# Kernel optimization log

Measured on AMD Instinct MI355X. Metric: run time of the kernel, lower is better.

The kernel has to match this reference:

```python
import jax, jax.numpy as jnp
import numpy as np

B, S, E, H = 4, 2048, 1024, 16
D = E // H          # head_dim = 64
FF = 3 * E          # feedforward_expansion = 3
EPS = 1.1920929e-07  # torch fp32 RMSNorm default eps (finfo.eps)


def rmsnorm(x, w):
    ms = jnp.mean(jnp.square(x), axis=-1, keepdims=True)
    return x * jax.lax.rsqrt(ms + EPS) * w


def setup_inputs() -> dict:
    key = jax.random.key(0)
    ks = jax.random.split(key, 12)
    s = 0.02
    return {
        "x": jax.random.normal(ks[0], (B, S, E), dtype=jnp.float32),
        "mask": jnp.ones((B, 1, 1, S), dtype=jnp.int32),
        "Wq": jax.random.normal(ks[1], (E, E), dtype=jnp.float32) * s,
        "bq": jnp.zeros((E,), dtype=jnp.float32),
        "Wkv": jax.random.normal(ks[2], (E, 2 * E), dtype=jnp.float32) * s,
        "bkv": jnp.zeros((2 * E,), dtype=jnp.float32),
        "Wo": jax.random.normal(ks[3], (E, E), dtype=jnp.float32) * s,
        "bo": jnp.zeros((E,), dtype=jnp.float32),
        "norm1_w": jnp.ones((E,), dtype=jnp.float32),
        "norm3_w": jnp.ones((E,), dtype=jnp.float32),
        "W1": jax.random.normal(ks[4], (E, FF), dtype=jnp.float32) * s,
        "b1": jnp.zeros((FF,), dtype=jnp.float32),
        "W2": jax.random.normal(ks[5], (FF, E), dtype=jnp.float32) * s,
        "b2": jnp.zeros((E,), dtype=jnp.float32),
    }


def attention(xn, mask, Wq, bq, Wkv, bkv, Wo, bo):
    q = xn @ Wq + bq                         # [B,S,E]
    kv = xn @ Wkv + bkv                      # [B,S,2E]
    k, v = jnp.split(kv, 2, axis=-1)
    q = q.reshape(B, S, H, D).transpose(0, 2, 1, 3)   # [B,H,S,D]
    k = k.reshape(B, S, H, D).transpose(0, 2, 1, 3)
    v = v.reshape(B, S, H, D).transpose(0, 2, 1, 3)
    scores = jnp.einsum("bhqd,bhkd->bhqk", q, k) / jnp.sqrt(jnp.float32(D))
    scores = jnp.where(mask == 0, -jnp.inf, scores)
    probs = jax.nn.softmax(scores, axis=-1)
    out = jnp.einsum("bhqk,bhkd->bhqd", probs, v)     # [B,H,S,D]
    out = out.transpose(0, 2, 1, 3).reshape(B, S, E)
    return out @ Wo + bo


def reference(x, mask, Wq, bq, Wkv, bkv, Wo, bo, norm1_w, norm3_w, W1, b1, W2, b2):
    # self-attention sublayer (pre-norm, residual; dropout = identity in eval)
    xn = rmsnorm(x, norm1_w)
    x = x + attention(xn, mask, Wq, bq, Wkv, bkv, Wo, bo)
    # feedforward sublayer: Linear -> exact GELU -> Linear
    xn = rmsnorm(x, norm3_w)
    h = jax.nn.gelu(xn @ W1 + b1, approximate=False)
    x = x + (h @ W2 + b2)
    return x
```

## Files before the change

### kernel.cpp

```cpp
#include <hip/hip_runtime.h>
#include <stdint.h>
#include <math.h>

typedef unsigned short u16;
typedef __attribute__((ext_vector_type(8))) short short8;
typedef __attribute__((ext_vector_type(4))) float f32x4;
typedef __attribute__((ext_vector_type(16))) float f32x16;
typedef __attribute__((ext_vector_type(4))) u16 u16x4;
typedef __attribute__((ext_vector_type(4))) uint32_t u32x4;
typedef __attribute__((ext_vector_type(2))) uint32_t u32x2;
typedef __attribute__((ext_vector_type(2))) int int2v;

#define DEV static __device__ __forceinline__

constexpr int Bb = 4, Ss = 2048, Ee = 1024, Hh = 16;
constexpr int MR = Bb * Ss;
constexpr int QKS = 2048;
constexpr float EPSf = 1.1920929e-07f;
constexpr float C1 = 0.125f * 1.44269504088896340736f;

DEV u16 f2bf(float f) {
  uint32_t u = __float_as_uint(f);
  u += 0x7FFFu + ((u >> 16) & 1u);
  return (u16)(u >> 16);
}
DEV float gelu_exact(float v) { return 0.5f * v * (1.0f + erff(v * 0.70710678118654752440f)); }

DEV uint32_t pkbf(float lo, float hi) {
  uint32_t r;
  asm("v_cvt_pk_bf16_f32 %0, %1, %2" : "=v"(r) : "v"(lo), "v"(hi));
  return r;
}

DEV float fexp2(float x) {
  float r;
  asm("v_exp_f32 %0, %1" : "=v"(r) : "v"(x));
  return r;
}

typedef const __attribute__((address_space(1))) void* gas_cp;
typedef __attribute__((address_space(3))) void* las_p;

DEV void gload16(const void* g, void* l) {
  __builtin_amdgcn_global_load_lds((gas_cp)(uintptr_t)g,
                                   (las_p)(uint32_t)(uintptr_t)l, 16, 0, 0);
}

DEV float xchg32(float x, int lane) {
  int2v r = __builtin_amdgcn_permlane32_swap(__float_as_int(x), __float_as_int(x), false, false);
  return __int_as_float(lane < 32 ? r.x : r.y);
}

__global__ __launch_bounds__(256) void rmsnorm_kernel(const float* __restrict__ x,
                                                      const float* __restrict__ w,
                                                      u16* __restrict__ out) {
  const int row = blockIdx.x, tid = threadIdx.x;
  const float4 v = ((const float4*)(x + (size_t)row * Ee))[tid];
  float ss = v.x * v.x + v.y * v.y + v.z * v.z + v.w * v.w;
#pragma unroll
  for (int off = 1; off < 64; off <<= 1) ss += __shfl_xor(ss, off, 64);
  __shared__ float red[4];
  if ((tid & 63) == 0) red[tid >> 6] = ss;
  __syncthreads();
  const float total = red[0] + red[1] + red[2] + red[3];
  const float scale = rsqrtf(total * (1.0f / Ee) + EPSf);
  const float4 wv = ((const float4*)w)[tid];
  u16x4 o;
  o.x = f2bf(v.x * scale * wv.x);
  o.y = f2bf(v.y * scale * wv.y);
  o.z = f2bf(v.z * scale * wv.z);
  o.w = f2bf(v.w * scale * wv.w);
  ((u16x4*)(out + (size_t)row * Ee))[tid] = o;
}

__global__ __launch_bounds__(256) void transpose_cast_kernel(const float* __restrict__ in,
                                                             u16* __restrict__ out,
                                                             int R, int C) {
  __shared__ float t[32][33];
  const int c0 = blockIdx.x * 32, r0 = blockIdx.y * 32;
  const int tx = threadIdx.x, ty = threadIdx.y;
#pragma unroll
  for (int i = 0; i < 4; ++i)
    t[ty + i * 8][tx] = in[(size_t)(r0 + ty + i * 8) * C + c0 + tx];
  __syncthreads();
#pragma unroll
  for (int i = 0; i < 4; ++i) {
    const int cc = ty + i * 8;
    out[(size_t)(c0 + cc) * R + r0 + tx] = f2bf(t[tx][cc]);
  }
}

__global__ __launch_bounds__(256) void bias_concat_kernel(const float* __restrict__ bq,
                                                          const float* __restrict__ bkv,
                                                          float* __restrict__ o) {
  const int i = blockIdx.x * 256 + threadIdx.x;
  o[i] = (i < 1024) ? bq[i] : bkv[i - 1024];
}

template <int EPI>
__global__ __launch_bounds__(512, 2) void gemm_kernel(const u16* __restrict__ A,
                                                      const u16* __restrict__ Bt,
                                                      const float* __restrict__ bias,
                                                      const float* __restrict__ resid,
                                                      void* __restrict__ outp,
                                                      int M, int N, int K) {
  constexpr int SLOT = 24576;
  __shared__ alignas(16) u16 lds[3 * SLOT];
  const int tid = threadIdx.x, lane = tid & 63, wave = tid >> 6;
  const int wr = wave >> 1, wc = wave & 1;
  const int nwg = (int)(gridDim.x * gridDim.y);
  int lin = (int)(blockIdx.y * gridDim.x + blockIdx.x);
  lin = (lin & 7) * (nwg >> 3) + (lin >> 3);
  const int bx = lin % (int)gridDim.x, by = lin / (int)gridDim.x;
  const int m0 = by * 256, n0 = bx * 128;
  const int l4 = lane >> 4, l15 = lane & 15, l7q = l15 & 7;
  const int srow = lane >> 3;
  const int sw = ((lane & 7) ^ srow) * 8;

  const u16* gsrc[6];
  uint32_t ldst[6];
#pragma unroll
  for (int g = 0; g < 4; ++g) {
    const int c = g * 8 + wave;
    gsrc[g] = A + (size_t)(m0 + c * 8 + srow) * K + sw;
    ldst[g] = c * 512;
  }
#pragma unroll
  for (int g = 0; g < 2; ++g) {
    const int c = g * 8 + wave;
    gsrc[4 + g] = Bt + (size_t)(n0 + c * 8 + srow) * K + sw;
    ldst[4 + g] = 16384 + c * 512;
  }

  const int ktiles = K >> 6;
  auto stage = [&](int t) {
    const uint32_t sbase = (uint32_t)(t % 3) * SLOT;
#pragma unroll
    for (int u = 0; u < 6; ++u)
      gload16(gsrc[u] + t * 64, (void*)&lds[sbase + ldst[u]]);
  };

  f32x4 acc[4][4];
#pragma unroll
  for (int i = 0; i < 4; ++i)
#pragma unroll
    for (int j = 0; j < 4; ++j) acc[i][j] = f32x4{0.f, 0.f, 0.f, 0.f};

  stage(0);
  stage(1);
  for (int t = 0; t < ktiles; ++t) {
    __builtin_amdgcn_sched_barrier(0);
    if (t + 1 < ktiles) asm volatile("s_waitcnt vmcnt(6)" ::: "memory");
    else                asm volatile("s_waitcnt vmcnt(0)" ::: "memory");
    __builtin_amdgcn_s_barrier();
    __builtin_amdgcn_sched_barrier(0);
    if (t + 2 < ktiles) stage(t + 2);

    const u16* sa = &lds[(t % 3) * SLOT];
    const u16* sb = sa + 16384;
    short8 af[2][4], bf[2][4];
#pragma unroll
    for (int kk2 = 0; kk2 < 2; ++kk2) {
#pragma unroll
      for (int i = 0; i < 4; ++i)
        af[kk2][i] = *(const short8*)&sa[(wr * 64 + i * 16 + l15) * 64 +
                                         (((kk2 * 4 + l4) ^ l7q) * 8)];
#pragma unroll
      for (int j = 0; j < 4; ++j)
        bf[kk2][j] = *(const short8*)&sb[(wc * 64 + j * 16 + l15) * 64 +
                                         (((kk2 * 4 + l4) ^ l7q) * 8)];
    }
    __builtin_amdgcn_s_setprio(1);
#pragma unroll
    for (int kk2 = 0; kk2 < 2; ++kk2)
#pragma unroll
      for (int i = 0; i < 4; ++i)
#pragma unroll
        for (int j = 0; j < 4; ++j)
          acc[i][j] = __builtin_amdgcn_mfma_f32_16x16x32_bf16(af[kk2][i], bf[kk2][j],
                                                              acc[i][j], 0, 0, 0);
    __builtin_amdgcn_s_setprio(0);
  }

  const int rbase = m0 + wr * 64, cbase = n0 + wc * 64;
#pragma unroll
  for (int i = 0; i < 4; ++i) {
#pragma unroll
    for (int reg = 0; reg < 4; ++reg) {
      const int row = rbase + i * 16 + l4 * 4 + reg;
#pragma unroll
      for (int j = 0; j < 4; ++j) {
        const int col = cbase + j * 16 + l15;
        float v = acc[i][j][reg];
        if constexpr (EPI == 0) {
          v += bias[col];
          ((u16*)outp)[(size_t)row * N + col] = f2bf(v);
        } else if constexpr (EPI == 1) {
          v += bias[row];
          ((u16*)outp)[(size_t)row * N + col] = f2bf(v);
        } else if constexpr (EPI == 2) {
          v += bias[col] + resid[(size_t)row * N + col];
          ((float*)outp)[(size_t)row * N + col] = v;
        } else {
          v += bias[col];
          ((u16*)outp)[(size_t)row * N + col] = f2bf(gelu_exact(v));
        }
      }
    }
  }
}

__global__ __launch_bounds__(256, 4) void attn_kernel(const u16* __restrict__ qk,
                                                      const u16* __restrict__ vT,
                                                      u16* __restrict__ o) {
  __shared__ alignas(16) u16 Ks[2][64 * 64];
  __shared__ alignas(16) u16 Vs[2][64 * 64];

  const int tid = threadIdx.x, lane = tid & 63, wave = tid >> 6;
  const int bh = blockIdx.x, b = bh >> 4, h = bh & 15;
  const int q0 = blockIdx.y * 128;
  const int l31 = lane & 31, hi = lane >> 5, l7 = lane & 7;
  const int srow = lane >> 3;
  const int sw = ((lane & 7) ^ srow) * 8;

  const u16* qbase = qk + (size_t)(b * Ss + q0 + wave * 32 + l31) * QKS + h * 64;
  short8 qf[4];
#pragma unroll
  for (int ds = 0; ds < 4; ++ds)
    qf[ds] = *(const short8*)&qbase[ds * 16 + hi * 8];

  short8 ones;
#pragma unroll
  for (int i = 0; i < 8; ++i) ones[i] = (short)0x3F80;

  f32x16 accO[2];
  f32x16 accS;
#pragma unroll
  for (int dt = 0; dt < 2; ++dt)
#pragma unroll
    for (int r = 0; r < 16; ++r) accO[dt][r] = 0.f;
#pragma unroll
  for (int r = 0; r < 16; ++r) accS[r] = 0.f;
  float m = -INFINITY;

  const size_t krowbase = (size_t)(b * Ss) * QKS + 1024 + h * 64;
  const size_t vrowbase = (size_t)(h * 64) * MR + b * Ss;

  auto stage = [&](int buf, int kv0) {
#pragma unroll
    for (int c = 0; c < 4; ++c) {
      const int g = wave * 4 + c;
      if (g < 8) {
        const int r = g * 8 + srow;
        gload16(&qk[krowbase + (size_t)(kv0 + r) * QKS + sw], &Ks[buf][g * 512]);
      } else {
        const int gg = g - 8;
        const int dr = gg * 8 + srow;
        gload16(&vT[vrowbase + (size_t)dr * MR + kv0 + sw], &Vs[buf][gg * 512]);
      }
    }
  };

  stage(0, 0);
  constexpr int NT = Ss / 64;
  for (int t = 0; t < NT; ++t) {
    const int cur = t & 1;
    __syncthreads();
    if (t + 1 < NT) stage(cur ^ 1, (t + 1) * 64);

    f32x16 sct[2];
#pragma unroll
    for (int t2 = 0; t2 < 2; ++t2)
#pragma unroll
      for (int r = 0; r < 16; ++r) sct[t2][r] = 0.f;
#pragma unroll
    for (int ds = 0; ds < 4; ++ds) {
#pragma unroll
      for (int t2 = 0; t2 < 2; ++t2) {
        const short8 kf = *(const short8*)&Ks[cur][(t2 * 32 + l31) * 64 + (((ds * 2 + hi) ^ l7) * 8)];
        sct[t2] = __builtin_amdgcn_mfma_f32_32x32x16_bf16(kf, qf[ds], sct[t2], 0, 0, 0);
      }
    }

    float mx = fmaxf(sct[0][0], sct[0][1]);
#pragma unroll
    for (int r = 2; r < 16; r += 2) mx = fmaxf(fmaxf(mx, sct[0][r]), sct[0][r + 1]);
#pragma unroll
    for (int r = 0; r < 16; r += 2) mx = fmaxf(fmaxf(mx, sct[1][r]), sct[1][r + 1]);
    const float rowmax = fmaxf(mx, xchg32(mx, lane));

    if (__any(rowmax > m + 64.f)) {
      const float mnew = fmaxf(m, rowmax);
      const float corr = fexp2((m - mnew) * C1);
      m = mnew;
      accS[0] *= corr;
#pragma unroll
      for (int dt = 0; dt < 2; ++dt)
#pragma unroll
        for (int r = 0; r < 16; ++r) accO[dt][r] *= corr;
    }
    const float negmC = -m * C1;

#pragma unroll
    for (int t2 = 0; t2 < 2; ++t2) {
      float pv[16];
#pragma unroll
      for (int r = 0; r < 16; ++r) pv[r] = fexp2(fmaf(sct[t2][r], C1, negmC));
#pragma unroll
      for (int s2 = 0; s2 < 2; ++s2) {
        const uint32_t w0 = pkbf(pv[s2 * 8 + 0], pv[s2 * 8 + 1]);
        const uint32_t w1 = pkbf(pv[s2 * 8 + 2], pv[s2 * 8 + 3]);
        const uint32_t w2 = pkbf(pv[s2 * 8 + 4], pv[s2 * 8 + 5]);
        const uint32_t w3 = pkbf(pv[s2 * 8 + 6], pv[s2 * 8 + 7]);
        const int2v a = __builtin_amdgcn_permlane32_swap((int)w2, (int)w0, false, false);
        const int2v c = __builtin_amdgcn_permlane32_swap((int)w3, (int)w1, false, false);
        u32x4 fw; fw.x = (uint32_t)a.y; fw.y = (uint32_t)c.y; fw.z = (uint32_t)a.x; fw.w = (uint32_t)c.x;
        const short8 pf = *(const short8*)&fw;
        const int cb = (t2 * 2 + s2) * 2 + hi;
#pragma unroll
        for (int dt = 0; dt < 2; ++dt) {
          const short8 vf = *(const short8*)&Vs[cur][(dt * 32 + l31) * 64 + ((cb ^ l7) * 8)];
          accO[dt] = __builtin_amdgcn_mfma_f32_32x32x16_bf16(vf, pf, accO[dt], 0, 0, 0);
        }
        accS = __builtin_amdgcn_mfma_f32_32x32x16_bf16(ones, pf, accS, 0, 0, 0);
      }
    }
  }

  const float inv = 1.0f / accS[0];
  u16* obase = o + (size_t)(b * Ss + q0 + wave * 32 + l31) * Ee + h * 64;
#pragma unroll
  for (int dt = 0; dt < 2; ++dt) {
#pragma unroll
    for (int g4 = 0; g4 < 4; ++g4) {
      const int d0 = dt * 32 + g4 * 8 + 4 * hi;
      u32x2 w;
      w.x = pkbf(accO[dt][g4 * 4 + 0] * inv, accO[dt][g4 * 4 + 1] * inv);
      w.y = pkbf(accO[dt][g4 * 4 + 2] * inv, accO[dt][g4 * 4 + 3] * inv);
      *(u32x2*)&obase[d0] = w;
    }
  }
}

extern "C" void kernel_launch(void* const* d_in, const int* in_sizes, int n_in,
                              void* d_out, int out_size, void* d_ws, size_t ws_size,
                              hipStream_t stream) {
  const float* x   = (const float*)d_in[0];
  const float* Wq  = (const float*)d_in[2];
  const float* bq  = (const float*)d_in[3];
  const float* Wkv = (const float*)d_in[4];
  const float* bkv = (const float*)d_in[5];
  const float* Wo  = (const float*)d_in[6];
  const float* bo  = (const float*)d_in[7];
  const float* n1w = (const float*)d_in[8];
  const float* n3w = (const float*)d_in[9];
  const float* W1  = (const float*)d_in[10];
  const float* b1  = (const float*)d_in[11];
  const float* W2  = (const float*)d_in[12];
  const float* b2  = (const float*)d_in[13];
  float* out = (float*)d_out;

  char* p = (char*)d_ws;
  auto alloc = [&](size_t elems) { u16* r = (u16*)p; p += elems * sizeof(u16); return r; };
  u16* Wqt  = alloc((size_t)1024 * 1024);
  u16* Wkvt = alloc((size_t)2048 * 1024);
  u16* Wot  = alloc((size_t)1024 * 1024);
  u16* W1t  = alloc((size_t)3072 * 1024);
  u16* W2t  = alloc((size_t)1024 * 3072);
  u16* xn   = alloc((size_t)MR * 1024);
  u16* qkb  = alloc((size_t)MR * 2048);
  u16* vT   = alloc((size_t)1024 * MR);
  u16* ao   = alloc((size_t)MR * 1024);
  u16* hb   = alloc((size_t)MR * 3072);
  float* biasQK = (float*)p;

  const dim3 tb(32, 8);
  transpose_cast_kernel<<<dim3(1024 / 32, 1024 / 32), tb, 0, stream>>>(Wq, Wqt, 1024, 1024);
  transpose_cast_kernel<<<dim3(2048 / 32, 1024 / 32), tb, 0, stream>>>(Wkv, Wkvt, 1024, 2048);
  transpose_cast_kernel<<<dim3(1024 / 32, 1024 / 32), tb, 0, stream>>>(Wo, Wot, 1024, 1024);
  transpose_cast_kernel<<<dim3(3072 / 32, 1024 / 32), tb, 0, stream>>>(W1, W1t, 1024, 3072);
  transpose_cast_kernel<<<dim3(1024 / 32, 3072 / 32), tb, 0, stream>>>(W2, W2t, 3072, 1024);
  bias_concat_kernel<<<8, 256, 0, stream>>>(bq, bkv, biasQK);

  rmsnorm_kernel<<<MR, 256, 0, stream>>>(x, n1w, xn);

  gemm_kernel<0><<<dim3(2048 / 128, MR / 256), 512, 0, stream>>>(xn, Wqt, biasQK, nullptr, qkb, MR, 2048, 1024);
  gemm_kernel<1><<<dim3(MR / 128, 1024 / 256), 512, 0, stream>>>(Wkvt + (size_t)1024 * 1024, xn,
                                                                 bkv + 1024, nullptr, vT, 1024, MR, 1024);

  attn_kernel<<<dim3(Bb * Hh, Ss / 128), 256, 0, stream>>>(qkb, vT, ao);

  gemm_kernel<2><<<dim3(1024 / 128, MR / 256), 512, 0, stream>>>(ao, Wot, bo, x, out, MR, 1024, 1024);

  rmsnorm_kernel<<<MR, 256, 0, stream>>>(out, n3w, xn);

  gemm_kernel<3><<<dim3(3072 / 128, MR / 256), 512, 0, stream>>>(xn, W1t, b1, nullptr, hb, MR, 3072, 1024);
  gemm_kernel<2><<<dim3(1024 / 128, MR / 256), 512, 0, stream>>>(hb, W2t, b2, out, out, MR, 1024, 3072);
}
```

Baseline: 375.4 us.

## Restructure GEMM into 256-row tiles with double buffering and tanh-form GELU

Replaces the GEMM kernel with a templated version that uses 256-wide N tiles for the QK and W1 projections. It uses a 2x4 wave layout with 8 row fragments per wave and drops from triple to double LDS buffering with a simpler wait scheme. The larger tiles are meant to raise data reuse per LDS load and cut global traffic, at the cost of more accumulator registers and lower occupancy. The exact erf GELU is also swapped for a tanh-style approximation built on exp2 and a hardware reciprocal, which lowers epilogue cost but changes numerics slightly.

```diff
diff --git a/kernel.cpp b/kernel.cpp
--- a/kernel.cpp
+++ b/kernel.cpp
@@ -24,7 +24,6 @@
   u += 0x7FFFu + ((u >> 16) & 1u);
   return (u16)(u >> 16);
 }
-DEV float gelu_exact(float v) { return 0.5f * v * (1.0f + erff(v * 0.70710678118654752440f)); }
 
 DEV uint32_t pkbf(float lo, float hi) {
   uint32_t r;
@@ -36,6 +35,17 @@
   float r;
   asm("v_exp_f32 %0, %1" : "=v"(r) : "v"(x));
   return r;
+}
+DEV float frcp(float x) {
+  float r;
+  asm("v_rcp_f32 %0, %1" : "=v"(r) : "v"(x));
+  return r;
+}
+
+DEV float gelu_fast(float x) {
+  const float inner = x * fmaf(x * x, 0.044715f, 1.0f);
+  const float e = fexp2(inner * -2.3022082f);
+  return x * frcp(1.0f + e);
 }
 
 typedef const __attribute__((address_space(1))) void* gas_cp;
@@ -97,99 +107,102 @@
   o[i] = (i < 1024) ? bq[i] : bkv[i - 1024];
 }
 
-template <int EPI>
-__global__ __launch_bounds__(512, 2) void gemm_kernel(const u16* __restrict__ A,
-                                                      const u16* __restrict__ Bt,
-                                                      const float* __restrict__ bias,
-                                                      const float* __restrict__ resid,
-                                                      void* __restrict__ outp,
-                                                      int M, int N, int K) {
-  constexpr int SLOT = 24576;
-  __shared__ alignas(16) u16 lds[3 * SLOT];
+template <int BN, int EPI>
+__global__ __launch_bounds__(512) void gemm256(const u16* __restrict__ A,
+                                               const u16* __restrict__ Bt,
+                                               const float* __restrict__ bias,
+                                               const float* __restrict__ resid,
+                                               void* __restrict__ outp,
+                                               int M, int N, int K) {
+  constexpr int BM = 256, BK = 64;
+  constexpr int NF = BN / 64;
+  constexpr int ACH = 4;
+  constexpr int BCH = BN / 64;
+  constexpr int A_SZ = BM * BK;
+  constexpr int B_SZ = BN * BK;
+  constexpr int SLOT = A_SZ + B_SZ;
+  __shared__ alignas(16) u16 lds[2 * SLOT];
+
   const int tid = threadIdx.x, lane = tid & 63, wave = tid >> 6;
-  const int wr = wave >> 1, wc = wave & 1;
+  const int wr = wave >> 2, wc = wave & 3;
   const int nwg = (int)(gridDim.x * gridDim.y);
   int lin = (int)(blockIdx.y * gridDim.x + blockIdx.x);
   lin = (lin & 7) * (nwg >> 3) + (lin >> 3);
   const int bx = lin % (int)gridDim.x, by = lin / (int)gridDim.x;
-  const int m0 = by * 256, n0 = bx * 128;
+  const int m0 = by * BM, n0 = bx * BN;
   const int l4 = lane >> 4, l15 = lane & 15, l7q = l15 & 7;
-  const int srow = lane >> 3;
-  const int sw = ((lane & 7) ^ srow) * 8;
-
-  const u16* gsrc[6];
-  uint32_t ldst[6];
-#pragma unroll
-  for (int g = 0; g < 4; ++g) {
-    const int c = g * 8 + wave;
-    gsrc[g] = A + (size_t)(m0 + c * 8 + srow) * K + sw;
-    ldst[g] = c * 512;
-  }
-#pragma unroll
-  for (int g = 0; g < 2; ++g) {
-    const int c = g * 8 + wave;
-    gsrc[4 + g] = Bt + (size_t)(n0 + c * 8 + srow) * K + sw;
-    ldst[4 + g] = 16384 + c * 512;
-  }
-
-  const int ktiles = K >> 6;
+
+  const int strow = tid >> 3;
+  const int scol = ((tid & 7) ^ (strow & 7)) * 8;
+  const u16* asrc[ACH];
+  const u16* bsrc[BCH];
+#pragma unroll
+  for (int c = 0; c < ACH; ++c) asrc[c] = A + (size_t)(m0 + c * 64 + strow) * K + scol;
+#pragma unroll
+  for (int c = 0; c < BCH; ++c) bsrc[c] = Bt + (size_t)(n0 + c * 64 + strow) * K + scol;
+  const uint32_t ldto = (uint32_t)tid * 8;
+
+  const int T = K >> 6;
   auto stage = [&](int t) {
-    const uint32_t sbase = (uint32_t)(t % 3) * SLOT;
-#pragma unroll
-    for (int u = 0; u < 6; ++u)
-      gload16(gsrc[u] + t * 64, (void*)&lds[sbase + ldst[u]]);
+    u16* base = &lds[(t & 1) * SLOT];
+#pragma unroll
+    for (int c = 0; c < ACH; ++c)
+      gload16(asrc[c] + t * 64, base + c * 4096 + ldto);
+#pragma unroll
+    for (int c = 0; c < BCH; ++c)
+      gload16(bsrc[c] + t * 64, base + A_SZ + c * 4096 + ldto);
   };
 
-  f32x4 acc[4][4];
-#pragma unroll
-  for (int i = 0; i < 4; ++i)
-#pragma unroll
-    for (int j = 0; j < 4; ++j) acc[i][j] = f32x4{0.f, 0.f, 0.f, 0.f};
+  f32x4 acc[8][NF];
+#pragma unroll
+  for (int i = 0; i < 8; ++i)
+#pragma unroll
+    for (int j = 0; j < NF; ++j) acc[i][j] = f32x4{0.f, 0.f, 0.f, 0.f};
 
   stage(0);
-  stage(1);
-  for (int t = 0; t < ktiles; ++t) {
-    __builtin_amdgcn_sched_barrier(0);
-    if (t + 1 < ktiles) asm volatile("s_waitcnt vmcnt(6)" ::: "memory");
-    else                asm volatile("s_waitcnt vmcnt(0)" ::: "memory");
+  for (int t = 0; t < T; ++t) {
     __builtin_amdgcn_s_barrier();
     __builtin_amdgcn_sched_barrier(0);
-    if (t + 2 < ktiles) stage(t + 2);
-
-    const u16* sa = &lds[(t % 3) * SLOT];
-    const u16* sb = sa + 16384;
-    short8 af[2][4], bf[2][4];
-#pragma unroll
-    for (int kk2 = 0; kk2 < 2; ++kk2) {
-#pragma unroll
-      for (int i = 0; i < 4; ++i)
-        af[kk2][i] = *(const short8*)&sa[(wr * 64 + i * 16 + l15) * 64 +
-                                         (((kk2 * 4 + l4) ^ l7q) * 8)];
-#pragma unroll
-      for (int j = 0; j < 4; ++j)
-        bf[kk2][j] = *(const short8*)&sb[(wc * 64 + j * 16 + l15) * 64 +
-                                         (((kk2 * 4 + l4) ^ l7q) * 8)];
-    }
-    __builtin_amdgcn_s_setprio(1);
-#pragma unroll
-    for (int kk2 = 0; kk2 < 2; ++kk2)
-#pragma unroll
-      for (int i = 0; i < 4; ++i)
-#pragma unroll
-        for (int j = 0; j < 4; ++j)
-          acc[i][j] = __builtin_amdgcn_mfma_f32_16x16x32_bf16(af[kk2][i], bf[kk2][j],
+    if (t + 1 < T) stage(t + 1);
+    __builtin_amdgcn_sched_barrier(0);
+    if (t + 1 < T) {
+      if constexpr (ACH + BCH == 8) asm volatile("s_waitcnt vmcnt(8)" ::: "memory");
+      else                          asm volatile("s_waitcnt vmcnt(6)" ::: "memory");
+    } else {
+      asm volatile("s_waitcnt vmcnt(0)" ::: "memory");
+    }
+    __builtin_amdgcn_sched_barrier(0);
+
+    const u16* sa = &lds[(t & 1) * SLOT];
+    const u16* sb = sa + A_SZ;
+#pragma unroll
+    for (int kk = 0; kk < 2; ++kk) {
+      short8 af[8], bf[NF];
+#pragma unroll
+      for (int i = 0; i < 8; ++i)
+        af[i] = *(const short8*)&sa[(wr * 128 + i * 16 + l15) * 64 +
+                                    (((kk * 4 + l4) ^ l7q) * 8)];
+#pragma unroll
+      for (int j = 0; j < NF; ++j)
+        bf[j] = *(const short8*)&sb[(wc * (BN / 4) + j * 16 + l15) * 64 +
+                                    (((kk * 4 + l4) ^ l7q) * 8)];
+#pragma unroll
+      for (int i = 0; i < 8; ++i)
+#pragma unroll
+        for (int j = 0; j < NF; ++j)
+          acc[i][j] = __builtin_amdgcn_mfma_f32_16x16x32_bf16(af[i], bf[j],
                                                               acc[i][j], 0, 0, 0);
-    __builtin_amdgcn_s_setprio(0);
+    }
   }
 
-  const int rbase = m0 + wr * 64, cbase = n0 + wc * 64;
-#pragma unroll
-  for (int i = 0; i < 4; ++i) {
+  const int rbase = m0 + wr * 128, cbase = n0 + wc * (BN / 4);
+#pragma unroll
+  for (int i = 0; i < 8; ++i) {
 #pragma unroll
     for (int reg = 0; reg < 4; ++reg) {
       const int row = rbase + i * 16 + l4 * 4 + reg;
 #pragma unroll
-      for (int j = 0; j < 4; ++j) {
+      for (int j = 0; j < NF; ++j) {
         const int col = cbase + j * 16 + l15;
         float v = acc[i][j][reg];
         if constexpr (EPI == 0) {
@@ -203,7 +216,7 @@
           ((float*)outp)[(size_t)row * N + col] = v;
         } else {
           v += bias[col];
-          ((u16*)outp)[(size_t)row * N + col] = f2bf(gelu_exact(v));
+          ((u16*)outp)[(size_t)row * N + col] = f2bf(gelu_fast(v));
         }
       }
     }
@@ -384,16 +397,16 @@
 
   rmsnorm_kernel<<<MR, 256, 0, stream>>>(x, n1w, xn);
 
-  gemm_kernel<0><<<dim3(2048 / 128, MR / 256), 512, 0, stream>>>(xn, Wqt, biasQK, nullptr, qkb, MR, 2048, 1024);
-  gemm_kernel<1><<<dim3(MR / 128, 1024 / 256), 512, 0, stream>>>(Wkvt + (size_t)1024 * 1024, xn,
-                                                                 bkv + 1024, nullptr, vT, 1024, MR, 1024);
+  gemm256<256, 0><<<dim3(2048 / 256, MR / 256), 512, 0, stream>>>(xn, Wqt, biasQK, nullptr, qkb, MR, 2048, 1024);
+  gemm256<128, 1><<<dim3(MR / 128, 1024 / 256), 512, 0, stream>>>(Wkvt + (size_t)1024 * 1024, xn,
+                                                                  bkv + 1024, nullptr, vT, 1024, MR, 1024);
 
   attn_kernel<<<dim3(Bb * Hh, Ss / 128), 256, 0, stream>>>(qkb, vT, ao);
 
-  gemm_kernel<2><<<dim3(1024 / 128, MR / 256), 512, 0, stream>>>(ao, Wot, bo, x, out, MR, 1024, 1024);
+  gemm256<128, 2><<<dim3(1024 / 128, MR / 256), 512, 0, stream>>>(ao, Wot, bo, x, out, MR, 1024, 1024);
 
   rmsnorm_kernel<<<MR, 256, 0, stream>>>(out, n3w, xn);
 
-  gemm_kernel<3><<<dim3(3072 / 128, MR / 256), 512, 0, stream>>>(xn, W1t, b1, nullptr, hb, MR, 3072, 1024);
-  gemm_kernel<2><<<dim3(1024 / 128, MR / 256), 512, 0, stream>>>(hb, W2t, b2, out, out, MR, 1024, 3072);
-}
+  gemm256<256, 3><<<dim3(3072 / 256, MR / 256), 512, 0, stream>>>(xn, W1t, b1, nullptr, hb, MR, 3072, 1024);
+  gemm256<128, 2><<<dim3(1024 / 128, MR / 256), 512, 0, stream>>>(hb, W2t, b2, out, out, MR, 1024, 3072);
+}
```

New measurement: 353.3 us. -5.9%, faster.
